# Performance work log

Hardware: AMD Instinct MI355X
Metric: run time of the kernel (lower is better)

The kernel has to match this reference:

```python
import jax, jax.numpy as jnp
import numpy as np

N_EMB = 512
EMB_DIM = 64
DECAY = 0.99
EPS = 1e-5


def setup_inputs() -> dict:
    key = jax.random.key(0)
    k1, k2 = jax.random.split(key)
    x = jax.random.normal(k1, (32, EMB_DIM, 64, 64), dtype=jnp.float32)
    weight = jax.random.uniform(k2, (EMB_DIM, N_EMB), dtype=jnp.float32)  # rd_init=True: torch.rand(emb_dim, n_emb)
    cluster_size = jnp.zeros((N_EMB,), dtype=jnp.float32)
    embed_avg = weight  # buffer initialized as embed.clone()
    return {"x": x, "weight": weight, "cluster_size": cluster_size, "embed_avg": embed_avg}


def reference(x, weight, cluster_size, embed_avg):
    B, D, H, W = x.shape
    n_emb = weight.shape[1]
    # (B, D, H, W) -> (N, D) tokens
    flat = jnp.transpose(x, (0, 2, 3, 1)).reshape(-1, D)
    dist = (jnp.sum(flat * flat, axis=1, keepdims=True)
            - 2.0 * (flat @ weight)
            + jnp.sum(weight * weight, axis=0)[None, :])
    argmin = jnp.argmin(dist, axis=1)                      # (N,)
    quant = jnp.take(weight.T, argmin, axis=0)             # gather -> (N, D)
    result = jnp.transpose(quant.reshape(B, H, W, D), (0, 3, 1, 2))  # (B, D, H, W)

    # --- EMA codebook update (training branch) ---
    ones = jnp.ones(argmin.shape, dtype=x.dtype)
    n_idx = jax.ops.segment_sum(ones, argmin, num_segments=n_emb)    # onehot.sum(0)
    n_idx = jnp.where(n_idx == 0, jnp.ones_like(n_idx), n_idx)       # clamp empty clusters to 1
    new_cluster_size = DECAY * cluster_size + (1.0 - DECAY) * n_idx
    embed_sum = jax.ops.segment_sum(flat, argmin, num_segments=n_emb).T  # flatten.T @ onehot -> (D, n_emb)
    new_embed_avg = DECAY * embed_avg + (1.0 - DECAY) * embed_sum
    n = jnp.sum(new_cluster_size)
    cs = (new_cluster_size + EPS) / (n + n_emb * EPS) * n
    new_weight = new_embed_avg / cs[None, :]

    return result, argmin.reshape(B, H, W), new_weight, new_cluster_size, new_embed_avg
```

## Files before the change

kernel.cpp:

```cpp
#include <hip/hip_runtime.h>

#define NEMB 512
#define EMB 64
#define BSTR 262144
#define DECAYF 0.99f
#define OMDF 0.01f
#define EPSF 1e-5f
#define GAP_T 0.006f
#define QCAP 32768

typedef __attribute__((ext_vector_type(8))) short bf16x8;
typedef __attribute__((ext_vector_type(4))) float f32x4;

__device__ __forceinline__ unsigned short f2bf(float f) {
    unsigned u = __float_as_uint(f);
    return (unsigned short)((u + 0x7FFFu + ((u >> 16) & 1u)) >> 16);
}
__device__ __forceinline__ float bf2f(unsigned short h) {
    return __uint_as_float(((unsigned)h) << 16);
}

__device__ __forceinline__ void gl2lds16(const void* g, void* l) {
    __builtin_amdgcn_global_load_lds(
        (const __attribute__((address_space(1))) unsigned int*)g,
        (__attribute__((address_space(3))) unsigned int*)l, 16, 0, 0);
}

__global__ void prep_kernel(const float* __restrict__ w,
                            unsigned short* __restrict__ wh, unsigned short* __restrict__ wl,
                            float* __restrict__ wsq,
                            float* __restrict__ cnt_ws, unsigned* __restrict__ gcnt) {
    int j = threadIdx.x;
    if (blockIdx.x < 8) {
        int d0 = blockIdx.x << 3;
        bf16x8 hb, lb;
#pragma unroll
        for (int i = 0; i < 8; ++i) {
            float v = w[(d0 + i) * NEMB + j];
            unsigned short h = f2bf(v);
            hb[i] = (short)h;
            lb[i] = (short)f2bf(v - bf2f(h));
        }
        *(bf16x8*)(wh + j * EMB + d0) = hb;
        *(bf16x8*)(wl + j * EMB + d0) = lb;
    } else {
        float s = 0.f;
#pragma unroll
        for (int d = 0; d < EMB; ++d) { float v = w[d * NEMB + j]; s = fmaf(v, v, s); }
        wsq[j] = s;
        cnt_ws[j] = 0.f;
        if (j == 0) *gcnt = 0u;
    }
}

#define UPD(S1, J1, S2, J2, s_, j_) do { \
    if (s_ < S1 || (s_ == S1 && j_ < J1)) { S2 = S1; J2 = J1; S1 = s_; J1 = j_; } \
    else if (s_ < S2 || (s_ == S2 && j_ < J2)) { S2 = s_; J2 = j_; } } while (0)

__global__ __launch_bounds__(512, 4) void vq_main(
    const float* __restrict__ x,
    const unsigned short* __restrict__ wh, const unsigned short* __restrict__ wl,
    const float* __restrict__ wsq,
    float* __restrict__ out_arg, unsigned* __restrict__ gcnt, int* __restrict__ queue)
{
    __shared__ __align__(16) unsigned char ubuf[32768];
    __shared__ float wsq_s[NEMB];

    float* xhf = (float*)ubuf;
    unsigned short* whq = (unsigned short*)ubuf;
    unsigned short* wlq = whq + 8192;

    const int tid = threadIdx.x;
    const int blk = blockIdx.x;
    const int b    = blk >> 4;
    const int hgrp = blk & 15;
    const int t0 = b * 4096 + hgrp * 256;
    const float* xbase = x + b * BSTR + hgrp * 256;

    const int lane = tid & 63;
    const int wave = tid >> 6;
    const int l15  = lane & 15;
    const int quad = lane >> 4;
    const int wbase = wave << 5;

#pragma unroll
    for (int it = 0; it < 4; ++it) {
        int d = wave + (it << 3);
        gl2lds16(xbase + d * 4096 + (lane << 2), xhf + d * 256);
    }
    wsq_s[tid] = wsq[tid];
    __syncthreads();

    bf16x8 ah[2][2], al[2][2];
    float sqa[2] = {0.f, 0.f};

#pragma unroll
    for (int mt = 0; mt < 2; ++mt) {
        int m = wbase + (mt << 4) + l15;
        int k0l = quad << 3;
        bf16x8 hh, ll;
#pragma unroll
        for (int i = 0; i < 8; ++i) {
            float v = xhf[(k0l + i) * 256 + m];
            sqa[mt] = fmaf(v, v, sqa[mt]);
            unsigned short h = f2bf(v);
            hh[i] = (short)h;
            ll[i] = (short)f2bf(v - bf2f(h));
        }
        ah[mt][0] = hh; al[mt][0] = ll;
    }
    __syncthreads();

#pragma unroll
    for (int it = 0; it < 4; ++it) {
        int d = wave + (it << 3);
        gl2lds16(xbase + (32 + d) * 4096 + (lane << 2), xhf + d * 256);
    }
    __syncthreads();

    float xq[2][4];
#pragma unroll
    for (int mt = 0; mt < 2; ++mt) {
        int m = wbase + (mt << 4) + l15;
        int k0l = quad << 3;
        bf16x8 hh, ll;
#pragma unroll
        for (int i = 0; i < 8; ++i) {
            float v = xhf[(k0l + i) * 256 + m];
            sqa[mt] = fmaf(v, v, sqa[mt]);
            unsigned short h = f2bf(v);
            hh[i] = (short)h;
            ll[i] = (short)f2bf(v - bf2f(h));
        }
        ah[mt][1] = hh; al[mt][1] = ll;
        float sq = sqa[mt];
        sq += __shfl_xor(sq, 16, 64);
        sq += __shfl_xor(sq, 32, 64);
#pragma unroll
        for (int r = 0; r < 4; ++r)
            xq[mt][r] = __shfl(sq, (quad << 2) + r, 64);
    }
    __syncthreads();

    float v1[2][4], v2[2][4];
    int   j1[2][4];
#pragma unroll
    for (int mt = 0; mt < 2; ++mt)
#pragma unroll
        for (int r = 0; r < 4; ++r) { v1[mt][r] = 3.4e38f; v2[mt][r] = 3.4e38f; j1[mt][r] = 0; }

    const int m7 = l15 & 7;
    const int s0off = ((quad ^ m7) << 3);
    const int s1off = (((4 | quad) ^ m7) << 3);

#pragma unroll
    for (int it = 0; it < 4; ++it) {
        int g0 = (wave << 6) + (it << 9);
        int arr = g0 >> 10;
        int win0 = g0 & 1023;
        int win = win0 + lane;
        int row = win >> 3, slot = win & 7;
        const unsigned short* src =
            (arr ? wl : wh) + row * EMB + ((slot ^ (row & 7)) << 3);
        gl2lds16(src, (arr ? wlq : whq) + (win0 << 3));
    }
    __syncthreads();

    for (int q = 0; q < 4; ++q) {
        const int nbase = q << 7;
#pragma unroll 2
        for (int it = 0; it < 8; ++it) {
            const int ib = ((it << 4) + l15) << 6;
            bf16x8 b0 = *(const bf16x8*)(whq + ib + s0off);
            bf16x8 b1 = *(const bf16x8*)(whq + ib + s1off);
            bf16x8 b2 = *(const bf16x8*)(wlq + ib + s0off);
            bf16x8 b3 = *(const bf16x8*)(wlq + ib + s1off);
            const int n = nbase + (it << 4) + l15;
            float wq = wsq_s[n];

            f32x4 acc0 = (f32x4){0.f, 0.f, 0.f, 0.f};
            f32x4 acc1 = (f32x4){0.f, 0.f, 0.f, 0.f};
            acc0 = __builtin_amdgcn_mfma_f32_16x16x32_bf16(ah[0][0], b0, acc0, 0, 0, 0);
            acc1 = __builtin_amdgcn_mfma_f32_16x16x32_bf16(ah[1][0], b0, acc1, 0, 0, 0);
            acc0 = __builtin_amdgcn_mfma_f32_16x16x32_bf16(ah[0][1], b1, acc0, 0, 0, 0);
            acc1 = __builtin_amdgcn_mfma_f32_16x16x32_bf16(ah[1][1], b1, acc1, 0, 0, 0);
            acc0 = __builtin_amdgcn_mfma_f32_16x16x32_bf16(ah[0][0], b2, acc0, 0, 0, 0);
            acc1 = __builtin_amdgcn_mfma_f32_16x16x32_bf16(ah[1][0], b2, acc1, 0, 0, 0);
            acc0 = __builtin_amdgcn_mfma_f32_16x16x32_bf16(ah[0][1], b3, acc0, 0, 0, 0);
            acc1 = __builtin_amdgcn_mfma_f32_16x16x32_bf16(ah[1][1], b3, acc1, 0, 0, 0);
            acc0 = __builtin_amdgcn_mfma_f32_16x16x32_bf16(al[0][0], b0, acc0, 0, 0, 0);
            acc1 = __builtin_amdgcn_mfma_f32_16x16x32_bf16(al[1][0], b0, acc1, 0, 0, 0);
            acc0 = __builtin_amdgcn_mfma_f32_16x16x32_bf16(al[0][1], b1, acc0, 0, 0, 0);
            acc1 = __builtin_amdgcn_mfma_f32_16x16x32_bf16(al[1][1], b1, acc1, 0, 0, 0);

#pragma unroll
            for (int r = 0; r < 4; ++r) {
                float s0 = fmaf(-2.f, acc0[r], xq[0][r] + wq);
                bool p0 = s0 < v1[0][r];
                float mx0 = fmaxf(s0, v1[0][r]);
                v1[0][r] = fminf(s0, v1[0][r]);
                v2[0][r] = fminf(v2[0][r], mx0);
                j1[0][r] = p0 ? n : j1[0][r];

                float s1 = fmaf(-2.f, acc1[r], xq[1][r] + wq);
                bool p1 = s1 < v1[1][r];
                float mx1 = fmaxf(s1, v1[1][r]);
                v1[1][r] = fminf(s1, v1[1][r]);
                v2[1][r] = fminf(v2[1][r], mx1);
                j1[1][r] = p1 ? n : j1[1][r];
            }
        }
        __syncthreads();
        if (q < 3) {
#pragma unroll
            for (int it = 0; it < 4; ++it) {
                int g0 = (wave << 6) + (it << 9);
                int arr = g0 >> 10;
                int win0 = g0 & 1023;
                int win = win0 + lane;
                int row = win >> 3, slot = win & 7;
                const unsigned short* src =
                    (arr ? wl : wh) + (((q + 1) << 7) + row) * EMB + ((slot ^ (row & 7)) << 3);
                gl2lds16(src, (arr ? wlq : whq) + (win0 << 3));
            }
            __syncthreads();
        }
    }

#pragma unroll
    for (int mt = 0; mt < 2; ++mt)
#pragma unroll
        for (int r = 0; r < 4; ++r) {
            float a1 = v1[mt][r], a2 = v2[mt][r];
            int   aj = j1[mt][r];
#pragma unroll
            for (int msk = 1; msk < 16; msk <<= 1) {
                float o1 = __shfl_xor(a1, msk, 64);
                int   oj = __shfl_xor(aj, msk, 64);
                float o2 = __shfl_xor(a2, msk, 64);
                bool take = (o1 < a1) || (o1 == a1 && oj < aj);
                float mx = fmaxf(a1, o1);
                a2 = fminf(fminf(a2, o2), mx);
                a1 = fminf(a1, o1);
                aj = take ? oj : aj;
            }
            v1[mt][r] = a1; v2[mt][r] = a2; j1[mt][r] = aj;
        }

    if (l15 == 0) {
#pragma unroll
        for (int mt = 0; mt < 2; ++mt)
#pragma unroll
            for (int r = 0; r < 4; ++r) {
                int gt = t0 + wbase + (mt << 4) + (quad << 2) + r;
                out_arg[gt] = (float)j1[mt][r];
                if (v2[mt][r] - v1[mt][r] < GAP_T) {
                    unsigned idx = atomicAdd(gcnt, 1u);
                    if (idx < QCAP) queue[idx] = gt;
                }
            }
    }
}

__global__ __launch_bounds__(256) void refine_kernel(
    const float* __restrict__ x, const float* __restrict__ w,
    const float* __restrict__ wsq, const unsigned* __restrict__ gcnt,
    const int* __restrict__ queue, float* __restrict__ out_arg)
{
    __shared__ float wsq_s[NEMB];
    const int tid = threadIdx.x;
    wsq_s[tid] = wsq[tid];
    wsq_s[tid + 256] = wsq[tid + 256];
    __syncthreads();

    unsigned nfu = *gcnt;
    const int nf = (int)(nfu < (unsigned)QCAP ? nfu : (unsigned)QCAP);
    const int lane = tid & 63;
    const int gw = (blockIdx.x << 2) + (tid >> 6);

    for (int i = gw; i < nf; i += 1024) {
        const int t = queue[i] & 131071;
        const int b = t >> 12, pos = t & 4095;
        float xd = x[b * BSTR + lane * 4096 + pos];
        float xqv = xd * xd;
#pragma unroll
        for (int mk = 1; mk < 64; mk <<= 1) xqv += __shfl_xor(xqv, mk, 64);

        float accv[8];
#pragma unroll
        for (int k = 0; k < 8; ++k) accv[k] = 0.f;
#pragma unroll 4
        for (int d = 0; d < EMB; ++d) {
            float4 wa = *(const float4*)(w + d * NEMB + (lane << 2));
            float4 wb = *(const float4*)(w + d * NEMB + 256 + (lane << 2));
            float xv = __shfl(xd, d, 64);
            accv[0] = fmaf(xv, wa.x, accv[0]);
            accv[1] = fmaf(xv, wa.y, accv[1]);
            accv[2] = fmaf(xv, wa.z, accv[2]);
            accv[3] = fmaf(xv, wa.w, accv[3]);
            accv[4] = fmaf(xv, wb.x, accv[4]);
            accv[5] = fmaf(xv, wb.y, accv[5]);
            accv[6] = fmaf(xv, wb.z, accv[6]);
            accv[7] = fmaf(xv, wb.w, accv[7]);
        }

        float S1 = 3.4e38f, S2 = 3.4e38f; int J1 = 0, J2 = 0;
#pragma unroll
        for (int k = 0; k < 8; ++k) {
            int j = (k < 4) ? ((lane << 2) + k) : (256 + (lane << 2) + k - 4);
            float s = (xqv - 2.f * accv[k]) + wsq_s[j];
            UPD(S1, J1, S2, J2, s, j);
        }
#pragma unroll
        for (int mk = 1; mk < 64; mk <<= 1) {
            float os1 = __shfl_xor(S1, mk, 64); int oj1 = __shfl_xor(J1, mk, 64);
            float os2 = __shfl_xor(S2, mk, 64); int oj2 = __shfl_xor(J2, mk, 64);
            UPD(S1, J1, S2, J2, os1, oj1);
            UPD(S1, J1, S2, J2, os2, oj2);
        }

        int jm = J1;
        if (S2 - S1 < 1e-3f) {
            float w1 = w[lane * NEMB + J1];
            float w2 = w[lane * NEMB + J2];
            double e1 = (double)w1 * (double)w1 - 2.0 * (double)xd * (double)w1;
            double e2 = (double)w2 * (double)w2 - 2.0 * (double)xd * (double)w2;
#pragma unroll
            for (int mk = 1; mk < 64; mk <<= 1) {
                e1 += __shfl_xor(e1, mk, 64);
                e2 += __shfl_xor(e2, mk, 64);
            }
            if (e2 < e1 || (e2 == e1 && J2 < J1)) jm = J2;
        }
        if (lane == 0) out_arg[t] = (float)jm;
    }
}

__global__ __launch_bounds__(512, 4) void es_kernel(
    const float* __restrict__ x, const float* __restrict__ arg,
    float* __restrict__ es_p, float* __restrict__ cnt_ws)
{
    __shared__ unsigned short xh[16384];
    __shared__ int args_s[256];
    __shared__ float cacc[NEMB];

    const int tid = threadIdx.x;
    const int blk = blockIdx.x;
    const int flavor = blk & 1;
    const int chunk  = blk >> 1;
    const int b = chunk >> 3;
    const int tpos0 = (chunk & 7) << 9;

    cacc[tid] = 0.f;

    const int lane = tid & 63;
    const int wave = tid >> 6;
    const int l15  = lane & 15;
    const int quad = lane >> 4;
    const int jb   = wave << 5;

    f32x4 acc[4][2];
#pragma unroll
    for (int m = 0; m < 4; ++m)
#pragma unroll
        for (int nc = 0; nc < 2; ++nc) acc[m][nc] = (f32x4){0.f, 0.f, 0.f, 0.f};

    for (int st = 0; st < 2; ++st) {
        const int tpos = tpos0 + (st << 8);
#pragma unroll
        for (int it = 0; it < 8; ++it) {
            int idx = tid + (it << 9);
            int d = idx >> 6, q = idx & 63;
            float4 g = *(const float4*)(x + b * BSTR + d * 4096 + tpos + (q << 2));
            int c = q >> 1, half = q & 1;
            int off = d * 256 + ((c ^ (d & 7)) << 3) + (half << 2);
            ushort4 hv = {f2bf(g.x), f2bf(g.y), f2bf(g.z), f2bf(g.w)};
            *(ushort4*)(xh + off) = hv;
        }
        if (tid < 256) args_s[tid] = ((int)arg[b * 4096 + tpos + tid]) & 511;
        __syncthreads();

        if (flavor == 0 && tid < 256) atomicAdd(&cacc[args_s[tid]], 1.f);

#pragma unroll
        for (int kk = 0; kk < 8; ++kk) {
            bf16x8 a_[4];
#pragma unroll
            for (int m = 0; m < 4; ++m) {
                int d = (m << 4) + l15;
                int coff = ((((kk << 2) + quad) ^ (d & 7)) << 3);
                a_[m] = *(const bf16x8*)(xh + d * 256 + coff);
            }
            int argv[8];
            const int kb = (kk << 5) + (quad << 3);
#pragma unroll
            for (int i = 0; i < 8; ++i) argv[i] = args_s[kb + i];
#pragma unroll
            for (int nc = 0; nc < 2; ++nc) {
                const int jg = (flavor << 8) + jb + (nc << 4) + l15;
                bf16x8 bf;
#pragma unroll
                for (int i = 0; i < 8; ++i) bf[i] = (argv[i] == jg) ? (short)0x3F80 : (short)0;
#pragma unroll
                for (int m = 0; m < 4; ++m)
                    acc[m][nc] = __builtin_amdgcn_mfma_f32_16x16x32_bf16(a_[m], bf, acc[m][nc], 0, 0, 0);
            }
        }
        __syncthreads();
    }

    float* ep = es_p + blk * 16384;
#pragma unroll
    for (int m = 0; m < 4; ++m)
#pragma unroll
        for (int nc = 0; nc < 2; ++nc) {
            const int jl = jb + (nc << 4) + l15;
#pragma unroll
            for (int r = 0; r < 4; ++r) {
                const int d = (m << 4) + (quad << 2) + r;
                ep[d * 256 + jl] = acc[m][nc][r];
            }
        }
    if (flavor == 0) {
        float v = cacc[tid];
        if (v != 0.f) atomicAdd(&cnt_ws[tid], v);
    }
}

__global__ __launch_bounds__(256) void finalize_kernel(
    const float* __restrict__ cs_in, const float* __restrict__ avg_in,
    const float* __restrict__ cnt_ws, const float* __restrict__ es_p,
    float* __restrict__ out_w, float* __restrict__ out_ncs,
    float* __restrict__ out_avg) {
    __shared__ float red[256];
    const int tid = threadIdx.x;
    const int d  = blockIdx.x >> 1;
    const int jh = blockIdx.x & 1;

    float c0 = cnt_ws[tid], c1 = cnt_ws[tid + 256];
    float ncs0 = DECAYF * cs_in[tid] + OMDF * ((c0 == 0.f) ? 1.f : c0);
    float ncs1 = DECAYF * cs_in[tid + 256] + OMDF * ((c1 == 0.f) ? 1.f : c1);
    red[tid] = ncs0 + ncs1;
    __syncthreads();
    for (int s = 128; s > 0; s >>= 1) {
        if (tid < s) red[tid] += red[tid + s];
        __syncthreads();
    }
    const float n = red[0];

    const float* ep = es_p + jh * 16384 + d * 256 + tid;
    float s = 0.f;
#pragma unroll 16
    for (int c = 0; c < 256; ++c) s += ep[c * 32768];

    const float ncs = jh ? ncs1 : ncs0;
    const float csj = (ncs + EPSF) / (n + (float)NEMB * EPSF) * n;
    const int o = d * NEMB + (jh << 8) + tid;
    const float navg = DECAYF * avg_in[o] + OMDF * s;
    out_avg[o] = navg;
    out_w[o] = navg / csj;
    if (blockIdx.x == 0) { out_ncs[tid] = ncs0; out_ncs[tid + 256] = ncs1; }
}

__global__ __launch_bounds__(512) void result_kernel(
    const float* __restrict__ w, const float* __restrict__ arg,
    float* __restrict__ out_result)
{
    __shared__ float wrow8[8 * 512];
    const int tid = threadIdx.x;
    const int grp = blockIdx.x >> 6;
    const int chunk = blockIdx.x & 63;
#pragma unroll
    for (int d = 0; d < 8; ++d)
        wrow8[(d << 9) + tid] = w[((grp << 3) + d) * NEMB + tid];
    __syncthreads();

    const int t = (chunk << 11) + (tid << 2);
    const int o = (t >> 12) * BSTR + (t & 4095);
    float4 a4 = *(const float4*)(arg + t);
    int j0 = ((int)a4.x) & 511, j1 = ((int)a4.y) & 511;
    int j2 = ((int)a4.z) & 511, j3 = ((int)a4.w) & 511;
#pragma unroll
    for (int d = 0; d < 8; ++d) {
        const int dg = (grp << 3) + d;
        float4 r4 = {wrow8[(d << 9) + j0], wrow8[(d << 9) + j1],
                     wrow8[(d << 9) + j2], wrow8[(d << 9) + j3]};
        *(float4*)(out_result + o + dg * 4096) = r4;
    }
}

extern "C" void kernel_launch(void* const* d_in, const int* in_sizes, int n_in,
                              void* d_out, int out_size, void* d_ws, size_t ws_size,
                              hipStream_t stream) {
    (void)in_sizes; (void)n_in; (void)out_size; (void)ws_size;
    const float* x   = (const float*)d_in[0];
    const float* w   = (const float*)d_in[1];
    const float* cs  = (const float*)d_in[2];
    const float* avg = (const float*)d_in[3];

    float* out = (float*)d_out;
    float* out_result = out;
    float* out_arg    = out + 8388608;
    float* out_w      = out + 8519680;
    float* out_ncs    = out + 8552448;
    float* out_avg    = out + 8552960;
    float* es_p       = out;

    char* wsb = (char*)d_ws;
    unsigned short* wh = (unsigned short*)wsb;
    unsigned short* wl = (unsigned short*)(wsb + 65536);
    float* wsq      = (float*)(wsb + 131072);
    float* cnt_ws   = (float*)(wsb + 133120);
    unsigned* gcnt  = (unsigned*)(wsb + 135168);
    int* queue      = (int*)(wsb + 135232);

    prep_kernel<<<9, 512, 0, stream>>>(w, wh, wl, wsq, cnt_ws, gcnt);
    vq_main<<<512, 512, 0, stream>>>(x, wh, wl, wsq, out_arg, gcnt, queue);
    refine_kernel<<<256, 256, 0, stream>>>(x, w, wsq, gcnt, queue, out_arg);
    es_kernel<<<512, 512, 0, stream>>>(x, out_arg, es_p, cnt_ws);
    finalize_kernel<<<128, 256, 0, stream>>>(cs, avg, cnt_ws, es_p, out_w, out_ncs, out_avg);
    result_kernel<<<512, 512, 0, stream>>>(w, out_arg, out_result);
}
```

Before: 175.6 us.

## Halve vq_main token tile, double grid, raise occupancy and tighten refine gap

vq_main now handles 128 tokens per block (16 per wave) instead of 256, so the grid doubles to 1024 blocks and launch bounds request 8 blocks per CU. The whole 64-dim x tile is loaded in one pass, which removes the two-stage x load and its extra barriers, and one trailing barrier is dropped. The intent is more parallelism and latency hiding on the MFMA distance loop. In exchange each block reloads the full codebook for half as many tokens, doubling codebook LDS traffic per token. The refine gap threshold also shrinks sharply, so fewer tokens are queued for exact fp32 refinement, which risks argmin mismatches on near-ties.

```diff
diff --git a/kernel.cpp b/kernel.cpp
--- a/kernel.cpp
+++ b/kernel.cpp
@@ -6,7 +6,7 @@
 #define DECAYF 0.99f
 #define OMDF 0.01f
 #define EPSF 1e-5f
-#define GAP_T 0.006f
+#define GAP_T 4e-4f
 #define QCAP 32768
 
 typedef __attribute__((ext_vector_type(8))) short bf16x8;
@@ -57,7 +57,7 @@
     if (s_ < S1 || (s_ == S1 && j_ < J1)) { S2 = S1; J2 = J1; S1 = s_; J1 = j_; } \
     else if (s_ < S2 || (s_ == S2 && j_ < J2)) { S2 = s_; J2 = j_; } } while (0)
 
-__global__ __launch_bounds__(512, 4) void vq_main(
+__global__ __launch_bounds__(512, 8) void vq_main(
     const float* __restrict__ x,
     const unsigned short* __restrict__ wh, const unsigned short* __restrict__ wl,
     const float* __restrict__ wsq,
@@ -66,88 +66,65 @@
     __shared__ __align__(16) unsigned char ubuf[32768];
     __shared__ float wsq_s[NEMB];
 
-    float* xhf = (float*)ubuf;
+    float* xt = (float*)ubuf;
     unsigned short* whq = (unsigned short*)ubuf;
     unsigned short* wlq = whq + 8192;
 
     const int tid = threadIdx.x;
     const int blk = blockIdx.x;
-    const int b    = blk >> 4;
-    const int hgrp = blk & 15;
-    const int t0 = b * 4096 + hgrp * 256;
-    const float* xbase = x + b * BSTR + hgrp * 256;
+    const int b    = blk >> 5;
+    const int hgrp = blk & 31;
+    const int t0 = b * 4096 + hgrp * 128;
+    const float* xbase = x + b * BSTR + hgrp * 128;
 
     const int lane = tid & 63;
     const int wave = tid >> 6;
+
+#pragma unroll
+    for (int it = 0; it < 4; ++it) {
+        int ch = wave + (it << 3);
+        int d0 = ch << 1;
+        gl2lds16(xbase + (d0 + (lane >> 5)) * 4096 + ((lane & 31) << 2),
+                 xt + d0 * 128);
+    }
+    wsq_s[tid] = wsq[tid];
+    __syncthreads();
+
     const int l15  = lane & 15;
     const int quad = lane >> 4;
-    const int wbase = wave << 5;
-
-#pragma unroll
-    for (int it = 0; it < 4; ++it) {
-        int d = wave + (it << 3);
-        gl2lds16(xbase + d * 4096 + (lane << 2), xhf + d * 256);
-    }
-    wsq_s[tid] = wsq[tid];
-    __syncthreads();
-
-    bf16x8 ah[2][2], al[2][2];
-    float sqa[2] = {0.f, 0.f};
-
-#pragma unroll
-    for (int mt = 0; mt < 2; ++mt) {
-        int m = wbase + (mt << 4) + l15;
-        int k0l = quad << 3;
-        bf16x8 hh, ll;
-#pragma unroll
-        for (int i = 0; i < 8; ++i) {
-            float v = xhf[(k0l + i) * 256 + m];
-            sqa[mt] = fmaf(v, v, sqa[mt]);
-            unsigned short h = f2bf(v);
-            hh[i] = (short)h;
-            ll[i] = (short)f2bf(v - bf2f(h));
-        }
-        ah[mt][0] = hh; al[mt][0] = ll;
-    }
-    __syncthreads();
-
-#pragma unroll
-    for (int it = 0; it < 4; ++it) {
-        int d = wave + (it << 3);
-        gl2lds16(xbase + (32 + d) * 4096 + (lane << 2), xhf + d * 256);
-    }
-    __syncthreads();
-
-    float xq[2][4];
-#pragma unroll
-    for (int mt = 0; mt < 2; ++mt) {
-        int m = wbase + (mt << 4) + l15;
-        int k0l = quad << 3;
-        bf16x8 hh, ll;
-#pragma unroll
-        for (int i = 0; i < 8; ++i) {
-            float v = xhf[(k0l + i) * 256 + m];
-            sqa[mt] = fmaf(v, v, sqa[mt]);
-            unsigned short h = f2bf(v);
-            hh[i] = (short)h;
-            ll[i] = (short)f2bf(v - bf2f(h));
-        }
-        ah[mt][1] = hh; al[mt][1] = ll;
-        float sq = sqa[mt];
+    const int wbase = wave << 4;
+
+    bf16x8 ah[2], al[2];
+    float xq[4];
+    {
+        int m = wbase + l15;
+        float sq = 0.f;
+#pragma unroll
+        for (int ks = 0; ks < 2; ++ks) {
+            int k0 = (ks << 5) + (quad << 3);
+            bf16x8 hh, ll;
+#pragma unroll
+            for (int i = 0; i < 8; ++i) {
+                float v = xt[(k0 + i) * 128 + m];
+                sq = fmaf(v, v, sq);
+                unsigned short h = f2bf(v);
+                hh[i] = (short)h;
+                ll[i] = (short)f2bf(v - bf2f(h));
+            }
+            ah[ks] = hh; al[ks] = ll;
+        }
         sq += __shfl_xor(sq, 16, 64);
         sq += __shfl_xor(sq, 32, 64);
 #pragma unroll
         for (int r = 0; r < 4; ++r)
-            xq[mt][r] = __shfl(sq, (quad << 2) + r, 64);
-    }
-    __syncthreads();
-
-    float v1[2][4], v2[2][4];
-    int   j1[2][4];
-#pragma unroll
-    for (int mt = 0; mt < 2; ++mt)
-#pragma unroll
-        for (int r = 0; r < 4; ++r) { v1[mt][r] = 3.4e38f; v2[mt][r] = 3.4e38f; j1[mt][r] = 0; }
+            xq[r] = __shfl(sq, (quad << 2) + r, 64);
+    }
+    __syncthreads();
+
+    float v1[4], v2[4];
+    int   j1[4];
+#pragma unroll
+    for (int r = 0; r < 4; ++r) { v1[r] = 3.4e38f; v2[r] = 3.4e38f; j1[r] = 0; }
 
     const int m7 = l15 & 7;
     const int s0off = ((quad ^ m7) << 3);
@@ -178,40 +155,28 @@
             const int n = nbase + (it << 4) + l15;
             float wq = wsq_s[n];
 
-            f32x4 acc0 = (f32x4){0.f, 0.f, 0.f, 0.f};
-            f32x4 acc1 = (f32x4){0.f, 0.f, 0.f, 0.f};
-            acc0 = __builtin_amdgcn_mfma_f32_16x16x32_bf16(ah[0][0], b0, acc0, 0, 0, 0);
-            acc1 = __builtin_amdgcn_mfma_f32_16x16x32_bf16(ah[1][0], b0, acc1, 0, 0, 0);
-            acc0 = __builtin_amdgcn_mfma_f32_16x16x32_bf16(ah[0][1], b1, acc0, 0, 0, 0);
-            acc1 = __builtin_amdgcn_mfma_f32_16x16x32_bf16(ah[1][1], b1, acc1, 0, 0, 0);
-            acc0 = __builtin_amdgcn_mfma_f32_16x16x32_bf16(ah[0][0], b2, acc0, 0, 0, 0);
-            acc1 = __builtin_amdgcn_mfma_f32_16x16x32_bf16(ah[1][0], b2, acc1, 0, 0, 0);
-            acc0 = __builtin_amdgcn_mfma_f32_16x16x32_bf16(ah[0][1], b3, acc0, 0, 0, 0);
-            acc1 = __builtin_amdgcn_mfma_f32_16x16x32_bf16(ah[1][1], b3, acc1, 0, 0, 0);
-            acc0 = __builtin_amdgcn_mfma_f32_16x16x32_bf16(al[0][0], b0, acc0, 0, 0, 0);
-            acc1 = __builtin_amdgcn_mfma_f32_16x16x32_bf16(al[1][0], b0, acc1, 0, 0, 0);
-            acc0 = __builtin_amdgcn_mfma_f32_16x16x32_bf16(al[0][1], b1, acc0, 0, 0, 0);
-            acc1 = __builtin_amdgcn_mfma_f32_16x16x32_bf16(al[1][1], b1, acc1, 0, 0, 0);
+            f32x4 acc = (f32x4){0.f, 0.f, 0.f, 0.f};
+            acc = __builtin_amdgcn_mfma_f32_16x16x32_bf16(ah[0], b0, acc, 0, 0, 0);
+            acc = __builtin_amdgcn_mfma_f32_16x16x32_bf16(ah[1], b1, acc, 0, 0, 0);
+            acc = __builtin_amdgcn_mfma_f32_16x16x32_bf16(ah[0], b2, acc, 0, 0, 0);
+            acc = __builtin_amdgcn_mfma_f32_16x16x32_bf16(ah[1], b3, acc, 0, 0, 0);
+            acc = __builtin_amdgcn_mfma_f32_16x16x32_bf16(al[0], b0, acc, 0, 0, 0);
+            acc = __builtin_amdgcn_mfma_f32_16x16x32_bf16(al[1], b1, acc, 0, 0, 0);
+            acc = __builtin_amdgcn_mfma_f32_16x16x32_bf16(al[0], b2, acc, 0, 0, 0);
+            acc = __builtin_amdgcn_mfma_f32_16x16x32_bf16(al[1], b3, acc, 0, 0, 0);
 
 #pragma unroll
             for (int r = 0; r < 4; ++r) {
-                float s0 = fmaf(-2.f, acc0[r], xq[0][r] + wq);
-                bool p0 = s0 < v1[0][r];
-                float mx0 = fmaxf(s0, v1[0][r]);
-                v1[0][r] = fminf(s0, v1[0][r]);
-                v2[0][r] = fminf(v2[0][r], mx0);
-                j1[0][r] = p0 ? n : j1[0][r];
-
-                float s1 = fmaf(-2.f, acc1[r], xq[1][r] + wq);
-                bool p1 = s1 < v1[1][r];
-                float mx1 = fmaxf(s1, v1[1][r]);
-                v1[1][r] = fminf(s1, v1[1][r]);
-                v2[1][r] = fminf(v2[1][r], mx1);
-                j1[1][r] = p1 ? n : j1[1][r];
-            }
-        }
-        __syncthreads();
+                float s0 = fmaf(-2.f, acc[r], xq[r] + wq);
+                bool p0 = s0 < v1[r];
+                float mx0 = fmaxf(s0, v1[r]);
+                v1[r] = fminf(s0, v1[r]);
+                v2[r] = fminf(v2[r], mx0);
+                j1[r] = p0 ? n : j1[r];
+            }
+        }
         if (q < 3) {
+            __syncthreads();
 #pragma unroll
             for (int it = 0; it < 4; ++it) {
                 int g0 = (wave << 6) + (it << 9);
@@ -228,37 +193,33 @@
     }
 
 #pragma unroll
-    for (int mt = 0; mt < 2; ++mt)
+    for (int r = 0; r < 4; ++r) {
+        float a1 = v1[r], a2 = v2[r];
+        int   aj = j1[r];
+#pragma unroll
+        for (int msk = 1; msk < 16; msk <<= 1) {
+            float o1 = __shfl_xor(a1, msk, 64);
+            int   oj = __shfl_xor(aj, msk, 64);
+            float o2 = __shfl_xor(a2, msk, 64);
+            bool take = (o1 < a1) || (o1 == a1 && oj < aj);
+            float mx = fmaxf(a1, o1);
+            a2 = fminf(fminf(a2, o2), mx);
+            a1 = fminf(a1, o1);
+            aj = take ? oj : aj;
+        }
+        v1[r] = a1; v2[r] = a2; j1[r] = aj;
+    }
+
+    if (l15 == 0) {
 #pragma unroll
         for (int r = 0; r < 4; ++r) {
-            float a1 = v1[mt][r], a2 = v2[mt][r];
-            int   aj = j1[mt][r];
-#pragma unroll
-            for (int msk = 1; msk < 16; msk <<= 1) {
-                float o1 = __shfl_xor(a1, msk, 64);
-                int   oj = __shfl_xor(aj, msk, 64);
-                float o2 = __shfl_xor(a2, msk, 64);
-                bool take = (o1 < a1) || (o1 == a1 && oj < aj);
-                float mx = fmaxf(a1, o1);
-                a2 = fminf(fminf(a2, o2), mx);
-                a1 = fminf(a1, o1);
-                aj = take ? oj : aj;
-            }
-            v1[mt][r] = a1; v2[mt][r] = a2; j1[mt][r] = aj;
-        }
-
-    if (l15 == 0) {
-#pragma unroll
-        for (int mt = 0; mt < 2; ++mt)
-#pragma unroll
-            for (int r = 0; r < 4; ++r) {
-                int gt = t0 + wbase + (mt << 4) + (quad << 2) + r;
-                out_arg[gt] = (float)j1[mt][r];
-                if (v2[mt][r] - v1[mt][r] < GAP_T) {
-                    unsigned idx = atomicAdd(gcnt, 1u);
-                    if (idx < QCAP) queue[idx] = gt;
-                }
-            }
+            int gt = t0 + wbase + (quad << 2) + r;
+            out_arg[gt] = (float)j1[r];
+            if (v2[r] - v1[r] < GAP_T) {
+                unsigned idx = atomicAdd(gcnt, 1u);
+                if (idx < QCAP) queue[idx] = gt;
+            }
+        }
     }
 }
 
@@ -515,7 +476,7 @@
     int* queue      = (int*)(wsb + 135232);
 
     prep_kernel<<<9, 512, 0, stream>>>(w, wh, wl, wsq, cnt_ws, gcnt);
-    vq_main<<<512, 512, 0, stream>>>(x, wh, wl, wsq, out_arg, gcnt, queue);
+    vq_main<<<1024, 512, 0, stream>>>(x, wh, wl, wsq, out_arg, gcnt, queue);
     refine_kernel<<<256, 256, 0, stream>>>(x, w, wsq, gcnt, queue, out_arg);
     es_kernel<<<512, 512, 0, stream>>>(x, out_arg, es_p, cnt_ws);
     finalize_kernel<<<128, 256, 0, stream>>>(cs, avg, cnt_ws, es_p, out_w, out_ncs, out_avg);
```

Measured after the change: 238.4 us. 1.36x slower.
